# Optimization experiments

Measured on AMD Instinct MI355X. Metric: run time of the kernel, lower is better.

Reference implementation:

```python
import jax, jax.numpy as jnp
import numpy as np

D = 256
H = 8
DH = D // H
N = 100000
B = 256
T = 131072
HID_FUSE = 256   # fuse MLP hidden = d_model
HID_HEAD = 256   # QuantileHeads hidden
NQ = 3           # quantiles (q10, q50, q90)


def setup_inputs() -> dict:
    key = jax.random.key(0)
    ks = jax.random.split(key, 32)
    p = lambda k, *s: (0.02 * jax.random.normal(k, s, dtype=jnp.float32))
    inp = {
        'node_embeddings': jax.random.normal(ks[0], (N, D), dtype=jnp.float32),
        'target_index': jax.random.randint(ks[1], (B,), 0, N),
        'port_index': jax.random.randint(ks[2], (T,), 0, N),
        'port_batch': jnp.sort(jax.random.randint(ks[3], (T,), 0, B)),
        'port_weight': jax.random.uniform(ks[4], (T,), dtype=jnp.float32),
        # PMA pooling params (learnable seed + MHA projections, no biases)
        'seed': p(ks[5], D),
        'Wq_p': p(ks[6], D, D), 'Wk_p': p(ks[7], D, D), 'Wv_p': p(ks[8], D, D), 'Wo_p': p(ks[9], D, D),
        # target->portfolio cross-attention params
        'Wq_c': p(ks[10], D, D), 'Wk_c': p(ks[11], D, D), 'Wv_c': p(ks[12], D, D), 'Wo_c': p(ks[13], D, D),
        # fuse LayerNorm(3d) + MLP
        'ln_g': jnp.ones((3 * D,), jnp.float32), 'ln_b': jnp.zeros((3 * D,), jnp.float32),
        'fuse_W1': p(ks[14], 3 * D, HID_FUSE), 'fuse_b1': jnp.zeros((HID_FUSE,), jnp.float32),
        'fuse_W2': p(ks[15], HID_FUSE, D), 'fuse_b2': jnp.zeros((D,), jnp.float32),
        # quantile heads MLP
        'head_W1': p(ks[16], D, HID_HEAD), 'head_b1': jnp.zeros((HID_HEAD,), jnp.float32),
        'head_W2': p(ks[17], HID_HEAD, NQ), 'head_b2': jnp.zeros((NQ,), jnp.float32),
    }
    return inp


def _segment_attend(logits, v, seg, num_segments):
    # logits [T,H], v [T,H,DH], seg [T] -> pooled [num_segments, H, DH]
    m = jax.ops.segment_max(logits, seg, num_segments=num_segments)  # [B,H]
    e = jnp.exp(logits - m[seg])                                      # [T,H]
    s = jax.ops.segment_sum(e, seg, num_segments=num_segments)        # [B,H]
    p = e / (s[seg] + 1e-9)
    return jax.ops.segment_sum(p[..., None] * v, seg, num_segments=num_segments)


def reference(node_embeddings, target_index, port_index, port_batch, port_weight,
              seed, Wq_p, Wk_p, Wv_p, Wo_p, Wq_c, Wk_c, Wv_c, Wo_c,
              ln_g, ln_b, fuse_W1, fuse_b1, fuse_W2, fuse_b2,
              head_W1, head_b1, head_W2, head_b2):
    b = target_index.shape[0]
    scale = float(DH) ** -0.5
    tgt = node_embeddings[target_index]          # [B,D]
    tok = node_embeddings[port_index]            # [T,D]
    logw = jnp.log(port_weight + 1e-8)           # DV01 weighting as logit bias

    # --- PMA: learnable seed query pools DV01-weighted portfolio tokens ---
    q_p = (seed @ Wq_p).reshape(H, DH)
    k_p = (tok @ Wk_p).reshape(-1, H, DH)
    v_p = (tok @ Wv_p).reshape(-1, H, DH)
    lg_p = jnp.einsum('thd,hd->th', k_p, q_p) * scale + logw[:, None]
    pooled = _segment_attend(lg_p, v_p, port_batch, b).reshape(b, D)
    contexts = pooled @ Wo_p                     # [B,D]; zeros for empty portfolios

    # --- target -> portfolio cross-attention (residual) ---
    q_c = (tgt @ Wq_c).reshape(b, H, DH)
    k_c = (tok @ Wk_c).reshape(-1, H, DH)
    v_c = (tok @ Wv_c).reshape(-1, H, DH)
    lg_c = jnp.einsum('thd,thd->th', k_c, q_c[port_batch]) * scale + logw[:, None]
    att = _segment_attend(lg_c, v_c, port_batch, b).reshape(b, D)
    fused = tgt + att @ Wo_c                     # [B,D]; == tgt for empty portfolios

    # --- fuse: concat -> LN -> MLP ---
    z = jnp.concatenate([tgt, contexts, fused], axis=-1)  # [B,3D]
    mu = jnp.mean(z, axis=-1, keepdims=True)
    var = jnp.var(z, axis=-1, keepdims=True)
    z = (z - mu) * jax.lax.rsqrt(var + 1e-5) * ln_g + ln_b
    z = jax.nn.relu(z @ fuse_W1 + fuse_b1) @ fuse_W2 + fuse_b2  # [B,D]

    # --- quantile heads ---
    out = jax.nn.relu(z @ head_W1 + head_b1) @ head_W2 + head_b2  # [B,NQ]
    return out
```

## Files before the change

kernel.cpp:

```cpp
#include <hip/hip_runtime.h>
#include <hip/hip_bf16.h>

typedef __attribute__((ext_vector_type(8))) short short8;
typedef __attribute__((ext_vector_type(4))) float floatx4;

#define SCALE 0.17677669529663687f

__device__ __forceinline__ unsigned short f2bf(float f) {
  unsigned int x = __float_as_uint(f);
  x += 0x7fffu + ((x >> 16) & 1u);
  return (unsigned short)(x >> 16);
}
__device__ __forceinline__ float bf2f(unsigned short u) {
  return __uint_as_float(((unsigned int)u) << 16);
}

__global__ __launch_bounds__(256) void k_qc_gemm(
    const float* __restrict__ node, const int* __restrict__ tgt_idx,
    const float* __restrict__ seed,
    const float* __restrict__ Wq_c, const float* __restrict__ Wq_p,
    float* __restrict__ q_all, int B)
{
  __shared__ float act_l[4 * 256];
  const int tid = threadIdx.x;
  const int bt = blockIdx.x, nt = blockIdx.y;
  const int BT = B >> 2;
  for (int i = tid; i < 4 * 256; i += 256) {
    int m = i >> 8, k = i & 255;
    int b = bt * 4 + m;
    float v = 0.f;
    if (b < B)       v = node[(size_t)tgt_idx[b] * 256 + k];
    else if (b == B) v = seed[k];
    act_l[i] = v;
  }
  __syncthreads();
  const float* W = (bt == BT) ? Wq_p : Wq_c;
  const int m = tid >> 6, lane = tid & 63, ks = lane >> 4, n = lane & 15;
  const int n0 = nt * 16;
  float acc = 0.f;
  const float* Wp = W + (size_t)(ks * 64) * 256 + n0 + n;
  const float* ap = &act_l[m * 256 + ks * 64];
  #pragma unroll 8
  for (int k = 0; k < 64; ++k) acc += ap[k] * Wp[(size_t)k * 256];
  acc += __shfl_xor(acc, 16, 64);
  acc += __shfl_xor(acc, 32, 64);
  const int b = bt * 4 + m;
  if (ks == 0 && b <= B) q_all[(size_t)b * 256 + n0 + n] = acc;
}

__global__ __launch_bounds__(256) void k_fold(
    const float* __restrict__ Wk_c, const float* __restrict__ Wk_p,
    const float* __restrict__ q_all, const int* __restrict__ port_batch,
    unsigned short* __restrict__ u_c_all, unsigned short* __restrict__ u_p_t,
    int* __restrict__ seg, int T, int B)
{
  const int tid = threadIdx.x;
  const int bt = blockIdx.x, dt = blockIdx.y;
  const int BT = B >> 2;
  if (dt == 0) {
    int key = -1;
    if (bt < BT) { if (tid < 4) key = bt * 4 + tid; }
    else if (tid == 0) key = B;
    if (key >= 0) {
      int lo = 0, hi = T;
      while (lo < hi) { int mid = (lo + hi) >> 1; if (port_batch[mid] < key) lo = mid + 1; else hi = mid; }
      seg[key] = lo;
    }
  }
  const int m = tid >> 6, lane = tid & 63;
  const int b = bt * 4 + m;
  if (b > B) return;
  const float* Wk = (b == B) ? Wk_p : Wk_c;
  const float* q = q_all + (size_t)b * 256;
  #pragma unroll
  for (int t2 = 0; t2 < 2; ++t2) {
    const int idx = t2 * 64 + lane;
    const int h = idx >> 4;
    const int d = dt * 16 + (idx & 15);
    float acc = 0.f;
    const float* wr = Wk + (size_t)d * 256 + h * 32;
    const float* qr = q + h * 32;
    #pragma unroll 8
    for (int j = 0; j < 32; ++j) acc += wr[j] * qr[j];
    unsigned short v = f2bf(acc);
    if (b < B) u_c_all[(size_t)b * 2048 + h * 256 + d] = v;
    else       u_p_t[h * 256 + d] = v;
  }
}

__global__ __launch_bounds__(256, 3) void attn_kernel(
    const float* __restrict__ node,
    const int* __restrict__ port_index,
    const float* __restrict__ port_weight,
    const unsigned short* __restrict__ u_p_t,
    const unsigned short* __restrict__ u_c_all,
    const int* __restrict__ seg,
    float* __restrict__ slabs, int T, int S)
{
  __shared__ __align__(16) unsigned short tok_lds[64 * 264];
  __shared__ __align__(16) unsigned short E_t[16 * 72];
  __shared__ float l_lds[16];

  const int tid  = threadIdx.x;
  const int s    = blockIdx.x;
  const int b    = blockIdx.y;
  const int lane = tid & 63;
  const int w    = tid >> 6;
  const int q    = lane >> 4;
  const int n    = lane & 15;

  if (tid < 16) l_lds[tid] = 0.f;

  short8 ufrag[8];
  const unsigned short* ubase = (n < 8) ? (u_p_t + n * 256)
                                        : (u_c_all + (size_t)b * 2048 + (n - 8) * 256);
  #pragma unroll
  for (int s8 = 0; s8 < 8; ++s8)
    ufrag[s8] = *(const short8*)(ubase + q * 8 + s8 * 32);

  const int start  = seg[b];
  const int end    = seg[b + 1];
  const int ntiles = (end - start + 63) >> 6;

  floatx4 sacc[4];
  #pragma unroll
  for (int nt = 0; nt < 4; ++nt) sacc[nt] = (floatx4){0.f, 0.f, 0.f, 0.f};

  __syncthreads();

  for (int it = s; it < ntiles; it += S) {
    const int tbase = start + it * 64;
    {
      int t0 = tbase + w * 16 + n;
      int idxv = port_index[t0 < T ? t0 : T - 1];
      #pragma unroll
      for (int i = 0; i < 16; ++i) {
        int rb = __shfl(idxv, i, 64);
        floatx4 v = *(const floatx4*)(node + (size_t)rb * 256 + lane * 4);
        uint2 pk;
        asm("v_cvt_pk_bf16_f32 %0, %1, %2" : "=v"(pk.x) : "v"(v[0]), "v"(v[1]));
        asm("v_cvt_pk_bf16_f32 %0, %1, %2" : "=v"(pk.y) : "v"(v[2]), "v"(v[3]));
        const int row = w * 16 + i;
        const int swz = ((row >> 3) & 3) << 5;
        *(uint2*)((char*)(tok_lds + row * 264) + ((lane * 8) ^ swz)) = pk;
      }
    }
    float pw[4];
    #pragma unroll
    for (int r = 0; r < 4; ++r) { int tr = tbase + w * 16 + q * 4 + r; pw[r] = port_weight[tr < T ? tr : T - 1]; }

    floatx4 lacc = (floatx4){0.f, 0.f, 0.f, 0.f};
    {
      const int rowA = w * 16 + n;
      const char* abase = (const char*)(tok_lds + rowA * 264);
      const int swzA = ((rowA >> 3) & 3) << 5;
      #pragma unroll
      for (int k = 0; k < 8; ++k) {
        short8 af = *(const short8*)(abase + ((q * 16 + k * 64) ^ swzA));
        lacc = __builtin_amdgcn_mfma_f32_16x16x32_bf16(af, ufrag[k], lacc, 0, 0, 0);
      }
    }
    float lsum = 0.f;
    #pragma unroll
    for (int r = 0; r < 4; ++r) {
      const int tr = tbase + w * 16 + q * 4 + r;
      float e = 0.f;
      if (tr < end) {
        e = __expf(lacc[r] * SCALE) * (pw[r] + 1e-8f);
      }
      unsigned short eb = f2bf(e);
      E_t[n * 72 + w * 16 + q * 4 + r] = eb;
      lsum += bf2f(eb);
    }
    lsum += __shfl_xor(lsum, 16, 64);
    lsum += __shfl_xor(lsum, 32, 64);
    if (lane < 16) atomicAdd(&l_lds[lane], lsum);
    __syncthreads();
    short8 ea0 = *(const short8*)(E_t + n * 72 + q * 8);
    short8 ea1 = *(const short8*)(E_t + n * 72 + 32 + q * 8);
    const char* tbytes = (const char*)tok_lds;
    const int sq = q << 5;
    #pragma unroll
    for (int nt = 0; nt < 4; ++nt) {
      const int dx = ((w * 64 + nt * 16 + n) * 2) ^ sq;
      short8 b0, b1;
      #pragma unroll
      for (int j = 0; j < 8; ++j) b0[j] = *(const short*)(tbytes + (q * 8 + j) * 528 + dx);
      #pragma unroll
      for (int j = 0; j < 8; ++j) b1[j] = *(const short*)(tbytes + (32 + q * 8 + j) * 528 + dx);
      sacc[nt] = __builtin_amdgcn_mfma_f32_16x16x32_bf16(ea0, b0, sacc[nt], 0, 0, 0);
      sacc[nt] = __builtin_amdgcn_mfma_f32_16x16x32_bf16(ea1, b1, sacc[nt], 0, 0, 0);
    }
    __syncthreads();
  }

  float* stage = (float*)tok_lds;
  #pragma unroll
  for (int nt = 0; nt < 4; ++nt)
    #pragma unroll
    for (int r = 0; r < 4; ++r)
      stage[(q * 4 + r) * 256 + w * 64 + nt * 16 + n] = sacc[nt][r];
  __syncthreads();
  float* sl = slabs + ((size_t)b * S + s) * 4224;
  #pragma unroll
  for (int i = 0; i < 4; ++i) {
    const int row = i * 4 + w;
    const int c0 = (tid & 63) * 4;
    *(floatx4*)(sl + row * 256 + c0) = *(const floatx4*)(stage + row * 256 + c0);
  }
  if (tid < 16) sl[4096 + tid] = l_lds[tid];
}

__global__ __launch_bounds__(256) void k_slab_gemm(
    const float* __restrict__ slabs, int S,
    const float* __restrict__ Wv_p, const float* __restrict__ Wv_c,
    float* __restrict__ X)
{
  __shared__ float act_l[4 * 256];
  __shared__ float lsum[4];
  const int tid = threadIdx.x;
  const int bt = blockIdx.x, nt = blockIdx.y, z = blockIdx.z;
  const int head = nt >> 1;
  const int row = z * 8 + head;
  if (tid < 4) {
    const float* sl = slabs + (size_t)(bt * 4 + tid) * S * 4224;
    float l = 0.f;
    for (int s = 0; s < S; ++s) l += sl[s * 4224 + 4096 + row];
    lsum[tid] = 1.0f / (l + 1e-9f);
  }
  __syncthreads();
  for (int i = tid; i < 4 * 256; i += 256) {
    int m = i >> 8, k = i & 255;
    const float* sl = slabs + (size_t)(bt * 4 + m) * S * 4224;
    float sum = 0.f;
    for (int s = 0; s < S; ++s) sum += sl[s * 4224 + row * 256 + k];
    act_l[i] = sum * lsum[m];
  }
  __syncthreads();
  const int m = tid >> 6, lane = tid & 63, ks = lane >> 4, n = lane & 15;
  const int n0 = nt * 16;
  const float* W = z ? Wv_c : Wv_p;
  float acc = 0.f;
  const float* Wp = W + (size_t)(ks * 64) * 256 + n0 + n;
  const float* ap = &act_l[m * 256 + ks * 64];
  #pragma unroll 8
  for (int k = 0; k < 64; ++k) acc += ap[k] * Wp[(size_t)k * 256];
  acc += __shfl_xor(acc, 16, 64);
  acc += __shfl_xor(acc, 32, 64);
  if (ks == 0)
    X[(size_t)(bt * 4 + m) * 512 + z * 256 + n0 + n] = acc;
}

__global__ __launch_bounds__(256) void k_plain_gemm(
    const float* __restrict__ act, int act_ld,
    const float* __restrict__ W0, const float* __restrict__ W1,
    const float* __restrict__ bias0, const float* __restrict__ bias1,
    float* __restrict__ outp, int out_ld,
    int K, int relu)
{
  __shared__ float act_l[4 * 768];
  const int tid = threadIdx.x;
  const int bt = blockIdx.x, nt = blockIdx.y, z = blockIdx.z;
  const float* W = z ? W1 : W0;
  const float* bias = z ? bias1 : bias0;
  for (int i = tid; i < 4 * K; i += 256) {
    int m = i / K, k = i - m * K;
    act_l[m * K + k] = act[(size_t)(bt * 4 + m) * act_ld + z * K + k];
  }
  __syncthreads();
  const int m = tid >> 6, lane = tid & 63, ks = lane >> 4, n = lane & 15;
  const int n0 = nt * 16;
  const int Kq = K >> 2;
  float acc = 0.f;
  const float* Wp = W + (size_t)(ks * Kq) * 256 + n0 + n;
  const float* ap = &act_l[m * K + ks * Kq];
  #pragma unroll 8
  for (int k = 0; k < Kq; ++k) acc += ap[k] * Wp[(size_t)k * 256];
  acc += __shfl_xor(acc, 16, 64);
  acc += __shfl_xor(acc, 32, 64);
  if (ks == 0) {
    float v = acc + (bias ? bias[n0 + n] : 0.f);
    if (relu) v = fmaxf(v, 0.f);
    outp[(size_t)(bt * 4 + m) * out_ld + z * 256 + n0 + n] = v;
  }
}

__global__ __launch_bounds__(256) void k_ln_gemm(
    const float* __restrict__ node, const int* __restrict__ tgt_idx,
    const float* __restrict__ zbuf,
    const float* __restrict__ ln_g, const float* __restrict__ ln_b,
    const float* __restrict__ fuse_W1, const float* __restrict__ fuse_b1,
    float* __restrict__ h1)
{
  __shared__ float act_l[4 * 768];
  const int tid = threadIdx.x;
  const int bt = blockIdx.x, nt = blockIdx.y;
  for (int i = tid; i < 4 * 256; i += 256) {
    int m = i >> 8, k = i & 255;
    int b = bt * 4 + m;
    float tg = node[(size_t)tgt_idx[b] * 256 + k];
    float C  = zbuf[(size_t)b * 512 + k];
    float Fp = zbuf[(size_t)b * 512 + 256 + k];
    act_l[m * 768 + k]       = tg;
    act_l[m * 768 + 256 + k] = C;
    act_l[m * 768 + 512 + k] = tg + Fp;
  }
  __syncthreads();
  const int m = tid >> 6, lane = tid & 63;
  {
    float s = 0.f;
    for (int k = lane; k < 768; k += 64) s += act_l[m * 768 + k];
    #pragma unroll
    for (int o = 32; o >= 1; o >>= 1) s += __shfl_xor(s, o, 64);
    const float mu = s * (1.0f / 768.0f);
    float v = 0.f;
    for (int k = lane; k < 768; k += 64) { float d = act_l[m * 768 + k] - mu; v += d * d; }
    #pragma unroll
    for (int o = 32; o >= 1; o >>= 1) v += __shfl_xor(v, o, 64);
    const float rstd = 1.0f / sqrtf(v * (1.0f / 768.0f) + 1e-5f);
    for (int k = lane; k < 768; k += 64)
      act_l[m * 768 + k] = (act_l[m * 768 + k] - mu) * rstd * ln_g[k] + ln_b[k];
  }
  __syncthreads();
  const int ks = lane >> 4, n = lane & 15;
  const int n0 = nt * 16;
  float acc = 0.f;
  const float* Wp = fuse_W1 + (size_t)(ks * 192) * 256 + n0 + n;
  const float* ap = &act_l[m * 768 + ks * 192];
  #pragma unroll 8
  for (int k = 0; k < 192; ++k) acc += ap[k] * Wp[(size_t)k * 256];
  acc += __shfl_xor(acc, 16, 64);
  acc += __shfl_xor(acc, 32, 64);
  if (ks == 0)
    h1[(size_t)(bt * 4 + m) * 256 + n0 + n] = fmaxf(acc + fuse_b1[n0 + n], 0.f);
}

__global__ __launch_bounds__(256) void k_outhead(
    const float* __restrict__ hh, const float* __restrict__ head_W2,
    const float* __restrict__ head_b2, float* __restrict__ out)
{
  const int tid = threadIdx.x;
  const int m = tid >> 6, lane = tid & 63;
  const int b = blockIdx.x * 4 + m;
  float a0 = 0.f, a1 = 0.f, a2 = 0.f;
  for (int k = lane; k < 256; k += 64) {
    float h = hh[(size_t)b * 256 + k];
    a0 += h * head_W2[k * 3 + 0];
    a1 += h * head_W2[k * 3 + 1];
    a2 += h * head_W2[k * 3 + 2];
  }
  #pragma unroll
  for (int o = 32; o >= 1; o >>= 1) {
    a0 += __shfl_xor(a0, o, 64);
    a1 += __shfl_xor(a1, o, 64);
    a2 += __shfl_xor(a2, o, 64);
  }
  if (lane == 0) {
    out[b * 3 + 0] = a0 + head_b2[0];
    out[b * 3 + 1] = a1 + head_b2[1];
    out[b * 3 + 2] = a2 + head_b2[2];
  }
}

extern "C" void kernel_launch(void* const* d_in, const int* in_sizes, int n_in,
                              void* d_out, int out_size, void* d_ws, size_t ws_size,
                              hipStream_t stream) {
  const float* node        = (const float*)d_in[0];
  const int*   tgt_idx     = (const int*)d_in[1];
  const int*   port_index  = (const int*)d_in[2];
  const int*   port_batch  = (const int*)d_in[3];
  const float* port_weight = (const float*)d_in[4];
  const float* seed        = (const float*)d_in[5];
  const float* Wq_p = (const float*)d_in[6];
  const float* Wk_p = (const float*)d_in[7];
  const float* Wv_p = (const float*)d_in[8];
  const float* Wo_p = (const float*)d_in[9];
  const float* Wq_c = (const float*)d_in[10];
  const float* Wk_c = (const float*)d_in[11];
  const float* Wv_c = (const float*)d_in[12];
  const float* Wo_c = (const float*)d_in[13];
  const float* ln_g = (const float*)d_in[14];
  const float* ln_b = (const float*)d_in[15];
  const float* fuse_W1 = (const float*)d_in[16];
  const float* fuse_b1 = (const float*)d_in[17];
  const float* fuse_W2 = (const float*)d_in[18];
  const float* fuse_b2 = (const float*)d_in[19];
  const float* head_W1 = (const float*)d_in[20];
  const float* head_b1 = (const float*)d_in[21];
  const float* head_W2 = (const float*)d_in[22];
  const float* head_b2 = (const float*)d_in[23];

  const int B = in_sizes[1];
  const int T = in_sizes[2];

  char* ws = (char*)d_ws;
  unsigned short* u_p_t   = (unsigned short*)ws;
  int*            seg     = (int*)(ws + 4096);
  unsigned short* u_c_all = (unsigned short*)(ws + 8192);
  float* X    = (float*)(ws + 8192);
  float* zbuf = (float*)(ws + 8192 + (size_t)B * 2048);
  size_t slab_off = 8192 + (size_t)B * 4096;
  float* slabs = (float*)(ws + slab_off);
  float* h1 = slabs;
  float* z2 = h1 + (size_t)B * 256;
  float* hh = z2 + (size_t)B * 256;

  size_t per_slice = (size_t)B * 4224 * 4;
  int S = 1;
  if (ws_size > slab_off + per_slice) {
    size_t fit = (ws_size - slab_off - ((size_t)(B + 1) * 1024 + 4096)) / per_slice;
    S = (int)(fit < 1 ? 1 : (fit > 4 ? 4 : fit));
  }
  float* q_all = (float*)(ws + slab_off + (size_t)S * per_slice);

  const int BT = B / 4;

  k_qc_gemm<<<dim3(BT + 1, 16), 256, 0, stream>>>(node, tgt_idx, seed,
      Wq_c, Wq_p, q_all, B);
  k_fold<<<dim3(BT + 1, 16), 256, 0, stream>>>(Wk_c, Wk_p, q_all, port_batch,
      u_c_all, u_p_t, seg, T, B);
  attn_kernel<<<dim3(S, B), 256, 0, stream>>>(node, port_index, port_weight,
      u_p_t, u_c_all, seg, slabs, T, S);
  k_slab_gemm<<<dim3(BT, 16, 2), 256, 0, stream>>>(slabs, S, Wv_p, Wv_c, X);
  k_plain_gemm<<<dim3(BT, 16, 2), 256, 0, stream>>>(X, 512, Wo_p, Wo_c,
      nullptr, nullptr, zbuf, 512, 256, 0);
  k_ln_gemm<<<dim3(BT, 16), 256, 0, stream>>>(node, tgt_idx, zbuf,
      ln_g, ln_b, fuse_W1, fuse_b1, h1);
  k_plain_gemm<<<dim3(BT, 16, 1), 256, 0, stream>>>(h1, 256, fuse_W2, nullptr,
      fuse_b2, nullptr, z2, 256, 256, 0);
  k_plain_gemm<<<dim3(BT, 16, 1), 256, 0, stream>>>(z2, 256, head_W1, nullptr,
      head_b1, nullptr, hh, 256, 256, 1);
  k_outhead<<<BT, 256, 0, stream>>>(hh, head_W2, head_b2, (float*)d_out);
}
```

Measured before the change: 300.4 us.

## Fuse prep GEMMs into one kernel and tail MLP chain into one kernel

Result: slower. 586.2 us (+95.2%).

```diff
diff --git a/kernel.cpp b/kernel.cpp
--- a/kernel.cpp
+++ b/kernel.cpp
@@ -15,49 +15,22 @@
   return __uint_as_float(((unsigned int)u) << 16);
 }
 
-__global__ __launch_bounds__(256) void k_qc_gemm(
+__global__ __launch_bounds__(256) void k_prep(
     const float* __restrict__ node, const int* __restrict__ tgt_idx,
     const float* __restrict__ seed,
     const float* __restrict__ Wq_c, const float* __restrict__ Wq_p,
-    float* __restrict__ q_all, int B)
-{
-  __shared__ float act_l[4 * 256];
-  const int tid = threadIdx.x;
-  const int bt = blockIdx.x, nt = blockIdx.y;
-  const int BT = B >> 2;
-  for (int i = tid; i < 4 * 256; i += 256) {
-    int m = i >> 8, k = i & 255;
-    int b = bt * 4 + m;
-    float v = 0.f;
-    if (b < B)       v = node[(size_t)tgt_idx[b] * 256 + k];
-    else if (b == B) v = seed[k];
-    act_l[i] = v;
-  }
-  __syncthreads();
-  const float* W = (bt == BT) ? Wq_p : Wq_c;
-  const int m = tid >> 6, lane = tid & 63, ks = lane >> 4, n = lane & 15;
-  const int n0 = nt * 16;
-  float acc = 0.f;
-  const float* Wp = W + (size_t)(ks * 64) * 256 + n0 + n;
-  const float* ap = &act_l[m * 256 + ks * 64];
-  #pragma unroll 8
-  for (int k = 0; k < 64; ++k) acc += ap[k] * Wp[(size_t)k * 256];
-  acc += __shfl_xor(acc, 16, 64);
-  acc += __shfl_xor(acc, 32, 64);
-  const int b = bt * 4 + m;
-  if (ks == 0 && b <= B) q_all[(size_t)b * 256 + n0 + n] = acc;
-}
-
-__global__ __launch_bounds__(256) void k_fold(
     const float* __restrict__ Wk_c, const float* __restrict__ Wk_p,
-    const float* __restrict__ q_all, const int* __restrict__ port_batch,
+    const int* __restrict__ port_batch,
     unsigned short* __restrict__ u_c_all, unsigned short* __restrict__ u_p_t,
     int* __restrict__ seg, int T, int B)
 {
+  __shared__ float act_l[4][256];
+  __shared__ float q_l[4][256];
   const int tid = threadIdx.x;
-  const int bt = blockIdx.x, dt = blockIdx.y;
+  const int bt = blockIdx.x;
   const int BT = B >> 2;
-  if (dt == 0) {
+
+  {
     int key = -1;
     if (bt < BT) { if (tid < 4) key = bt * 4 + tid; }
     else if (tid == 0) key = B;
@@ -67,21 +40,43 @@
       seg[key] = lo;
     }
   }
+
   const int m = tid >> 6, lane = tid & 63;
   const int b = bt * 4 + m;
   if (b > B) return;
+
+  {
+    const float* src = (b < B) ? (node + (size_t)tgt_idx[b] * 256) : seed;
+    *(floatx4*)&act_l[m][lane * 4] = *(const floatx4*)(src + lane * 4);
+  }
+  const float* Wq = (b == B) ? Wq_p : Wq_c;
   const float* Wk = (b == B) ? Wk_p : Wk_c;
-  const float* q = q_all + (size_t)b * 256;
-  #pragma unroll
-  for (int t2 = 0; t2 < 2; ++t2) {
-    const int idx = t2 * 64 + lane;
-    const int h = idx >> 4;
-    const int d = dt * 16 + (idx & 15);
-    float acc = 0.f;
+
+  {
+    floatx4 acc = (floatx4){0.f, 0.f, 0.f, 0.f};
+    #pragma unroll 4
+    for (int k = 0; k < 256; ++k) {
+      float a = act_l[m][k];
+      floatx4 w = *(const floatx4*)(Wq + (size_t)k * 256 + lane * 4);
+      acc[0] += a * w[0]; acc[1] += a * w[1]; acc[2] += a * w[2]; acc[3] += a * w[3];
+    }
+    *(floatx4*)&q_l[m][lane * 4] = acc;
+  }
+
+  #pragma unroll 1
+  for (int r = 0; r < 32; ++r) {
+    const int h = r >> 2, d = (r & 3) * 64 + lane;
     const float* wr = Wk + (size_t)d * 256 + h * 32;
-    const float* qr = q + h * 32;
-    #pragma unroll 8
-    for (int j = 0; j < 32; ++j) acc += wr[j] * qr[j];
+    const float* qr = &q_l[m][h * 32];
+    floatx4 a4 = (floatx4){0.f, 0.f, 0.f, 0.f};
+    #pragma unroll
+    for (int j4 = 0; j4 < 8; ++j4) {
+      floatx4 w = *(const floatx4*)(wr + j4 * 4);
+      floatx4 qq = *(const floatx4*)(qr + j4 * 4);
+      a4[0] += w[0] * qq[0]; a4[1] += w[1] * qq[1];
+      a4[2] += w[2] * qq[2]; a4[3] += w[3] * qq[3];
+    }
+    float acc = (a4[0] + a4[1]) + (a4[2] + a4[3]);
     unsigned short v = f2bf(acc);
     if (b < B) u_c_all[(size_t)b * 2048 + h * 256 + d] = v;
     else       u_p_t[h * 256 + d] = v;
@@ -211,154 +206,164 @@
   if (tid < 16) sl[4096 + tid] = l_lds[tid];
 }
 
-__global__ __launch_bounds__(256) void k_slab_gemm(
+__global__ __launch_bounds__(256) void k_tail(
     const float* __restrict__ slabs, int S,
     const float* __restrict__ Wv_p, const float* __restrict__ Wv_c,
-    float* __restrict__ X)
-{
-  __shared__ float act_l[4 * 256];
-  __shared__ float lsum[4];
-  const int tid = threadIdx.x;
-  const int bt = blockIdx.x, nt = blockIdx.y, z = blockIdx.z;
-  const int head = nt >> 1;
-  const int row = z * 8 + head;
-  if (tid < 4) {
-    const float* sl = slabs + (size_t)(bt * 4 + tid) * S * 4224;
-    float l = 0.f;
-    for (int s = 0; s < S; ++s) l += sl[s * 4224 + 4096 + row];
-    lsum[tid] = 1.0f / (l + 1e-9f);
-  }
-  __syncthreads();
-  for (int i = tid; i < 4 * 256; i += 256) {
-    int m = i >> 8, k = i & 255;
-    const float* sl = slabs + (size_t)(bt * 4 + m) * S * 4224;
-    float sum = 0.f;
-    for (int s = 0; s < S; ++s) sum += sl[s * 4224 + row * 256 + k];
-    act_l[i] = sum * lsum[m];
-  }
-  __syncthreads();
-  const int m = tid >> 6, lane = tid & 63, ks = lane >> 4, n = lane & 15;
-  const int n0 = nt * 16;
-  const float* W = z ? Wv_c : Wv_p;
-  float acc = 0.f;
-  const float* Wp = W + (size_t)(ks * 64) * 256 + n0 + n;
-  const float* ap = &act_l[m * 256 + ks * 64];
-  #pragma unroll 8
-  for (int k = 0; k < 64; ++k) acc += ap[k] * Wp[(size_t)k * 256];
-  acc += __shfl_xor(acc, 16, 64);
-  acc += __shfl_xor(acc, 32, 64);
-  if (ks == 0)
-    X[(size_t)(bt * 4 + m) * 512 + z * 256 + n0 + n] = acc;
-}
-
-__global__ __launch_bounds__(256) void k_plain_gemm(
-    const float* __restrict__ act, int act_ld,
-    const float* __restrict__ W0, const float* __restrict__ W1,
-    const float* __restrict__ bias0, const float* __restrict__ bias1,
-    float* __restrict__ outp, int out_ld,
-    int K, int relu)
-{
-  __shared__ float act_l[4 * 768];
-  const int tid = threadIdx.x;
-  const int bt = blockIdx.x, nt = blockIdx.y, z = blockIdx.z;
-  const float* W = z ? W1 : W0;
-  const float* bias = z ? bias1 : bias0;
-  for (int i = tid; i < 4 * K; i += 256) {
-    int m = i / K, k = i - m * K;
-    act_l[m * K + k] = act[(size_t)(bt * 4 + m) * act_ld + z * K + k];
-  }
-  __syncthreads();
-  const int m = tid >> 6, lane = tid & 63, ks = lane >> 4, n = lane & 15;
-  const int n0 = nt * 16;
-  const int Kq = K >> 2;
-  float acc = 0.f;
-  const float* Wp = W + (size_t)(ks * Kq) * 256 + n0 + n;
-  const float* ap = &act_l[m * K + ks * Kq];
-  #pragma unroll 8
-  for (int k = 0; k < Kq; ++k) acc += ap[k] * Wp[(size_t)k * 256];
-  acc += __shfl_xor(acc, 16, 64);
-  acc += __shfl_xor(acc, 32, 64);
-  if (ks == 0) {
-    float v = acc + (bias ? bias[n0 + n] : 0.f);
-    if (relu) v = fmaxf(v, 0.f);
-    outp[(size_t)(bt * 4 + m) * out_ld + z * 256 + n0 + n] = v;
-  }
-}
-
-__global__ __launch_bounds__(256) void k_ln_gemm(
+    const float* __restrict__ Wo_p, const float* __restrict__ Wo_c,
     const float* __restrict__ node, const int* __restrict__ tgt_idx,
-    const float* __restrict__ zbuf,
     const float* __restrict__ ln_g, const float* __restrict__ ln_b,
     const float* __restrict__ fuse_W1, const float* __restrict__ fuse_b1,
-    float* __restrict__ h1)
+    const float* __restrict__ fuse_W2, const float* __restrict__ fuse_b2,
+    const float* __restrict__ head_W1, const float* __restrict__ head_b1,
+    const float* __restrict__ head_W2, const float* __restrict__ head_b2,
+    float* __restrict__ out)
 {
-  __shared__ float act_l[4 * 768];
-  const int tid = threadIdx.x;
-  const int bt = blockIdx.x, nt = blockIdx.y;
-  for (int i = tid; i < 4 * 256; i += 256) {
-    int m = i >> 8, k = i & 255;
-    int b = bt * 4 + m;
-    float tg = node[(size_t)tgt_idx[b] * 256 + k];
-    float C  = zbuf[(size_t)b * 512 + k];
-    float Fp = zbuf[(size_t)b * 512 + 256 + k];
-    act_l[m * 768 + k]       = tg;
-    act_l[m * 768 + 256 + k] = C;
-    act_l[m * 768 + 512 + k] = tg + Fp;
-  }
-  __syncthreads();
-  const int m = tid >> 6, lane = tid & 63;
-  {
-    float s = 0.f;
-    for (int k = lane; k < 768; k += 64) s += act_l[m * 768 + k];
-    #pragma unroll
-    for (int o = 32; o >= 1; o >>= 1) s += __shfl_xor(s, o, 64);
-    const float mu = s * (1.0f / 768.0f);
-    float v = 0.f;
-    for (int k = lane; k < 768; k += 64) { float d = act_l[m * 768 + k] - mu; v += d * d; }
-    #pragma unroll
-    for (int o = 32; o >= 1; o >>= 1) v += __shfl_xor(v, o, 64);
-    const float rstd = 1.0f / sqrtf(v * (1.0f / 768.0f) + 1e-5f);
-    for (int k = lane; k < 768; k += 64)
-      act_l[m * 768 + k] = (act_l[m * 768 + k] - mu) * rstd * ln_g[k] + ln_b[k];
-  }
-  __syncthreads();
-  const int ks = lane >> 4, n = lane & 15;
-  const int n0 = nt * 16;
-  float acc = 0.f;
-  const float* Wp = fuse_W1 + (size_t)(ks * 192) * 256 + n0 + n;
-  const float* ap = &act_l[m * 768 + ks * 192];
-  #pragma unroll 8
-  for (int k = 0; k < 192; ++k) acc += ap[k] * Wp[(size_t)k * 256];
-  acc += __shfl_xor(acc, 16, 64);
-  acc += __shfl_xor(acc, 32, 64);
-  if (ks == 0)
-    h1[(size_t)(bt * 4 + m) * 256 + n0 + n] = fmaxf(acc + fuse_b1[n0 + n], 0.f);
-}
-
-__global__ __launch_bounds__(256) void k_outhead(
-    const float* __restrict__ hh, const float* __restrict__ head_W2,
-    const float* __restrict__ head_b2, float* __restrict__ out)
-{
+  __shared__ float pooled_l[4][16][256];
+  __shared__ float X_l[4][512];
+  __shared__ float zv[4][768];
+  __shared__ float hbuf[4][256];
+  __shared__ float hbuf2[4][256];
+  __shared__ float linv[4][16];
+
   const int tid = threadIdx.x;
   const int m = tid >> 6, lane = tid & 63;
   const int b = blockIdx.x * 4 + m;
-  float a0 = 0.f, a1 = 0.f, a2 = 0.f;
-  for (int k = lane; k < 256; k += 64) {
-    float h = hh[(size_t)b * 256 + k];
-    a0 += h * head_W2[k * 3 + 0];
-    a1 += h * head_W2[k * 3 + 1];
-    a2 += h * head_W2[k * 3 + 2];
-  }
-  #pragma unroll
-  for (int o = 32; o >= 1; o >>= 1) {
-    a0 += __shfl_xor(a0, o, 64);
-    a1 += __shfl_xor(a1, o, 64);
-    a2 += __shfl_xor(a2, o, 64);
-  }
-  if (lane == 0) {
-    out[b * 3 + 0] = a0 + head_b2[0];
-    out[b * 3 + 1] = a1 + head_b2[1];
-    out[b * 3 + 2] = a2 + head_b2[2];
+  const float* sl0 = slabs + (size_t)b * S * 4224;
+
+  if (lane < 16) {
+    float l = 0.f;
+    for (int s = 0; s < S; ++s) l += sl0[s * 4224 + 4096 + lane];
+    linv[m][lane] = 1.0f / (l + 1e-9f);
+  }
+  #pragma unroll 1
+  for (int r = 0; r < 16; ++r) {
+    floatx4 p = (floatx4){0.f, 0.f, 0.f, 0.f};
+    for (int s = 0; s < S; ++s) {
+      floatx4 v = *(const floatx4*)(sl0 + s * 4224 + r * 256 + lane * 4);
+      p[0] += v[0]; p[1] += v[1]; p[2] += v[2]; p[3] += v[3];
+    }
+    const float iv = linv[m][r];
+    p[0] *= iv; p[1] *= iv; p[2] *= iv; p[3] *= iv;
+    *(floatx4*)&pooled_l[m][r][lane * 4] = p;
+  }
+
+  {
+    const int j = lane & 31, kh = lane >> 5;
+    #pragma unroll 1
+    for (int z = 0; z < 2; ++z) {
+      const float* Wv = z ? Wv_c : Wv_p;
+      #pragma unroll 1
+      for (int h = 0; h < 8; ++h) {
+        const float* pr = &pooled_l[m][z * 8 + h][kh * 128];
+        const float* wp = Wv + (size_t)(kh * 128) * 256 + h * 32 + j;
+        float a0 = 0.f, a1 = 0.f, a2 = 0.f, a3 = 0.f;
+        #pragma unroll 4
+        for (int kk = 0; kk < 128; kk += 4) {
+          a0 += pr[kk + 0] * wp[(size_t)(kk + 0) * 256];
+          a1 += pr[kk + 1] * wp[(size_t)(kk + 1) * 256];
+          a2 += pr[kk + 2] * wp[(size_t)(kk + 2) * 256];
+          a3 += pr[kk + 3] * wp[(size_t)(kk + 3) * 256];
+        }
+        float acc = (a0 + a1) + (a2 + a3);
+        acc += __shfl_xor(acc, 32, 64);
+        if (kh == 0) X_l[m][z * 256 + h * 32 + j] = acc;
+      }
+    }
+  }
+
+  floatx4 tg4 = *(const floatx4*)(node + (size_t)tgt_idx[b] * 256 + lane * 4);
+
+  #pragma unroll 1
+  for (int z = 0; z < 2; ++z) {
+    const float* Wo = z ? Wo_c : Wo_p;
+    floatx4 acc = (floatx4){0.f, 0.f, 0.f, 0.f};
+    #pragma unroll 4
+    for (int k = 0; k < 256; ++k) {
+      float a = X_l[m][z * 256 + k];
+      floatx4 w = *(const floatx4*)(Wo + (size_t)k * 256 + lane * 4);
+      acc[0] += a * w[0]; acc[1] += a * w[1]; acc[2] += a * w[2]; acc[3] += a * w[3];
+    }
+    if (z == 0) {
+      *(floatx4*)&zv[m][256 + lane * 4] = acc;
+    } else {
+      acc[0] += tg4[0]; acc[1] += tg4[1]; acc[2] += tg4[2]; acc[3] += tg4[3];
+      *(floatx4*)&zv[m][512 + lane * 4] = acc;
+    }
+  }
+  *(floatx4*)&zv[m][lane * 4] = tg4;
+
+  {
+    float sv = 0.f;
+    for (int k = lane; k < 768; k += 64) sv += zv[m][k];
+    #pragma unroll
+    for (int o = 32; o >= 1; o >>= 1) sv += __shfl_xor(sv, o, 64);
+    const float mu = sv * (1.0f / 768.0f);
+    float vv = 0.f;
+    for (int k = lane; k < 768; k += 64) { float d = zv[m][k] - mu; vv += d * d; }
+    #pragma unroll
+    for (int o = 32; o >= 1; o >>= 1) vv += __shfl_xor(vv, o, 64);
+    const float rstd = 1.0f / sqrtf(vv * (1.0f / 768.0f) + 1e-5f);
+    for (int k = lane; k < 768; k += 64)
+      zv[m][k] = (zv[m][k] - mu) * rstd * ln_g[k] + ln_b[k];
+  }
+
+  {
+    floatx4 acc = (floatx4){0.f, 0.f, 0.f, 0.f};
+    #pragma unroll 4
+    for (int k = 0; k < 768; ++k) {
+      float a = zv[m][k];
+      floatx4 w = *(const floatx4*)(fuse_W1 + (size_t)k * 256 + lane * 4);
+      acc[0] += a * w[0]; acc[1] += a * w[1]; acc[2] += a * w[2]; acc[3] += a * w[3];
+    }
+    floatx4 bb = *(const floatx4*)(fuse_b1 + lane * 4);
+    acc[0] = fmaxf(acc[0] + bb[0], 0.f); acc[1] = fmaxf(acc[1] + bb[1], 0.f);
+    acc[2] = fmaxf(acc[2] + bb[2], 0.f); acc[3] = fmaxf(acc[3] + bb[3], 0.f);
+    *(floatx4*)&hbuf[m][lane * 4] = acc;
+  }
+  {
+    floatx4 acc = (floatx4){0.f, 0.f, 0.f, 0.f};
+    #pragma unroll 4
+    for (int k = 0; k < 256; ++k) {
+      float a = hbuf[m][k];
+      floatx4 w = *(const floatx4*)(fuse_W2 + (size_t)k * 256 + lane * 4);
+      acc[0] += a * w[0]; acc[1] += a * w[1]; acc[2] += a * w[2]; acc[3] += a * w[3];
+    }
+    floatx4 bb = *(const floatx4*)(fuse_b2 + lane * 4);
+    acc[0] += bb[0]; acc[1] += bb[1]; acc[2] += bb[2]; acc[3] += bb[3];
+    *(floatx4*)&hbuf2[m][lane * 4] = acc;
+  }
+  {
+    floatx4 acc = (floatx4){0.f, 0.f, 0.f, 0.f};
+    #pragma unroll 4
+    for (int k = 0; k < 256; ++k) {
+      float a = hbuf2[m][k];
+      floatx4 w = *(const floatx4*)(head_W1 + (size_t)k * 256 + lane * 4);
+      acc[0] += a * w[0]; acc[1] += a * w[1]; acc[2] += a * w[2]; acc[3] += a * w[3];
+    }
+    floatx4 bb = *(const floatx4*)(head_b1 + lane * 4);
+    acc[0] = fmaxf(acc[0] + bb[0], 0.f); acc[1] = fmaxf(acc[1] + bb[1], 0.f);
+    acc[2] = fmaxf(acc[2] + bb[2], 0.f); acc[3] = fmaxf(acc[3] + bb[3], 0.f);
+    *(floatx4*)&hbuf[m][lane * 4] = acc;
+  }
+  {
+    float a0 = 0.f, a1 = 0.f, a2 = 0.f;
+    for (int k = lane; k < 256; k += 64) {
+      float h = hbuf[m][k];
+      a0 += h * head_W2[k * 3 + 0];
+      a1 += h * head_W2[k * 3 + 1];
+      a2 += h * head_W2[k * 3 + 2];
+    }
+    #pragma unroll
+    for (int o = 32; o >= 1; o >>= 1) {
+      a0 += __shfl_xor(a0, o, 64);
+      a1 += __shfl_xor(a1, o, 64);
+      a2 += __shfl_xor(a2, o, 64);
+    }
+    if (lane == 0) {
+      out[b * 3 + 0] = a0 + head_b2[0];
+      out[b * 3 + 1] = a1 + head_b2[1];
+      out[b * 3 + 2] = a2 + head_b2[2];
+    }
   }
 }
 
@@ -397,13 +402,8 @@
   unsigned short* u_p_t   = (unsigned short*)ws;
   int*            seg     = (int*)(ws + 4096);
   unsigned short* u_c_all = (unsigned short*)(ws + 8192);
-  float* X    = (float*)(ws + 8192);
-  float* zbuf = (float*)(ws + 8192 + (size_t)B * 2048);
   size_t slab_off = 8192 + (size_t)B * 4096;
   float* slabs = (float*)(ws + slab_off);
-  float* h1 = slabs;
-  float* z2 = h1 + (size_t)B * 256;
-  float* hh = z2 + (size_t)B * 256;
 
   size_t per_slice = (size_t)B * 4224 * 4;
   int S = 1;
@@ -411,24 +411,14 @@
     size_t fit = (ws_size - slab_off - ((size_t)(B + 1) * 1024 + 4096)) / per_slice;
     S = (int)(fit < 1 ? 1 : (fit > 4 ? 4 : fit));
   }
-  float* q_all = (float*)(ws + slab_off + (size_t)S * per_slice);
 
   const int BT = B / 4;
 
-  k_qc_gemm<<<dim3(BT + 1, 16), 256, 0, stream>>>(node, tgt_idx, seed,
-      Wq_c, Wq_p, q_all, B);
-  k_fold<<<dim3(BT + 1, 16), 256, 0, stream>>>(Wk_c, Wk_p, q_all, port_batch,
-      u_c_all, u_p_t, seg, T, B);
+  k_prep<<<dim3(BT + 1), 256, 0, stream>>>(node, tgt_idx, seed,
+      Wq_c, Wq_p, Wk_c, Wk_p, port_batch, u_c_all, u_p_t, seg, T, B);
   attn_kernel<<<dim3(S, B), 256, 0, stream>>>(node, port_index, port_weight,
       u_p_t, u_c_all, seg, slabs, T, S);
-  k_slab_gemm<<<dim3(BT, 16, 2), 256, 0, stream>>>(slabs, S, Wv_p, Wv_c, X);
-  k_plain_gemm<<<dim3(BT, 16, 2), 256, 0, stream>>>(X, 512, Wo_p, Wo_c,
-      nullptr, nullptr, zbuf, 512, 256, 0);
-  k_ln_gemm<<<dim3(BT, 16), 256, 0, stream>>>(node, tgt_idx, zbuf,
-      ln_g, ln_b, fuse_W1, fuse_b1, h1);
-  k_plain_gemm<<<dim3(BT, 16, 1), 256, 0, stream>>>(h1, 256, fuse_W2, nullptr,
-      fuse_b2, nullptr, z2, 256, 256, 0);
-  k_plain_gemm<<<dim3(BT, 16, 1), 256, 0, stream>>>(z2, 256, head_W1, nullptr,
-      head_b1, nullptr, hh, 256, 256, 1);
-  k_outhead<<<BT, 256, 0, stream>>>(hh, head_W2, head_b2, (float*)d_out);
-}
+  k_tail<<<dim3(BT), 256, 0, stream>>>(slabs, S, Wv_p, Wv_c, Wo_p, Wo_c,
+      node, tgt_idx, ln_g, ln_b, fuse_W1, fuse_b1, fuse_W2, fuse_b2,
+      head_W1, head_b1, head_W2, head_b2, (float*)d_out);
+}
```
